# Kernel tuning notes

Hardware: AMD Instinct MI355X
Metric: run time of the kernel (lower is better)

Reference implementation:

```python
import jax, jax.numpy as jnp
import numpy as np

N_NODES = 50000
N_EDGES = 800000
D = 128            # in_channels == hidden_channels
N_LAYERS = 3
OUT = 16
N_GRAPHS = 128


def setup_inputs() -> dict:
    key = jax.random.key(0)
    ks = jax.random.split(key, 12)
    x = jax.random.normal(ks[0], (N_NODES, D), dtype=jnp.float32)
    edge_index = jax.random.randint(ks[1], (2, N_EDGES), 0, N_NODES, dtype=jnp.int64)
    batch_ids = jnp.sort(jax.random.randint(ks[2], (N_NODES,), 0, N_GRAPHS, dtype=jnp.int64))
    s = 1.0 / np.sqrt(D)
    # Stacked per-layer GraphConv weights (all layers are D->D here).
    Wrel = jax.random.uniform(ks[3], (N_LAYERS, D, D), jnp.float32, -s, s)
    brel = jax.random.uniform(ks[4], (N_LAYERS, D), jnp.float32, -s, s)
    Wroot = jax.random.uniform(ks[5], (N_LAYERS, D, D), jnp.float32, -s, s)
    # post_mp MLP head
    W1 = jax.random.uniform(ks[6], (D, D), jnp.float32, -s, s)
    b1 = jax.random.uniform(ks[7], (D,), jnp.float32, -s, s)
    W2 = jax.random.uniform(ks[8], (D, OUT), jnp.float32, -s, s)
    b2 = jax.random.uniform(ks[9], (OUT,), jnp.float32, -s, s)
    return {"x": x, "edge_index": edge_index, "batch_ids": batch_ids,
            "Wrel": Wrel, "brel": brel, "Wroot": Wroot,
            "W1": W1, "b1": b1, "W2": W2, "b2": b2}


def reference(x, edge_index, batch_ids, Wrel, brel, Wroot, W1, b1, W2, b2):
    src, dst = edge_index[0], edge_index[1]
    h = x
    for l in range(N_LAYERS):
        # GraphConv: lin_rel(sum_{j->i} h_j) + lin_root(h_i)
        agg = jax.ops.segment_sum(h[src], dst, num_segments=N_NODES)  # [N, D]
        h = agg @ Wrel[l] + brel[l] + h @ Wroot[l]
        h = jax.nn.relu(h)
        # dropout p=0.0 / eval mode -> identity
    # global mean pool over graphs
    sums = jax.ops.segment_sum(h, batch_ids, num_segments=N_GRAPHS)          # [G, D]
    counts = jax.ops.segment_sum(jnp.ones((N_NODES,), h.dtype), batch_ids,
                                 num_segments=N_GRAPHS)                       # [G]
    pooled = sums / jnp.maximum(counts, 1.0)[:, None]
    # post_mp MLP (dropout identity in eval)
    out = (pooled @ W1 + b1) @ W2 + b2                                        # [G, OUT]
    return out
```

## Files before the change

kernel.cpp:

```cpp
#include <hip/hip_runtime.h>

#define N_NODES 50000
#define N_EDGES 800000
#define D 128
#define N_LAYERS 3
#define OUT_F 16
#define N_GRAPHS 128
#define NBUCK 391
#define EPB 4096
#define NB3 ((N_EDGES + EPB - 1) / EPB)
#define CAP 4096
#define NT32 ((N_NODES + 31) / 32)
#define PITCH 132
#define NCAST 6250
#define NPREPW 96

typedef __attribute__((ext_vector_type(8))) short short8;
typedef __attribute__((ext_vector_type(16))) float floatx16;

__device__ __forceinline__ unsigned short f2bf(float f) {
  unsigned int u = __float_as_uint(f);
  u += 0x7fff + ((u >> 16) & 1);
  return (unsigned short)(u >> 16);
}
__device__ __forceinline__ float bf2f(unsigned short b) {
  return __uint_as_float(((unsigned int)b) << 16);
}
__device__ __forceinline__ float blo(unsigned v) { return __uint_as_float(v << 16); }
__device__ __forceinline__ float bhi(unsigned v) { return __uint_as_float(v & 0xffff0000u); }

__global__ __launch_bounds__(256) void prep_part_kernel(
    const int* __restrict__ src, const int* __restrict__ dst,
    int* __restrict__ cursor, unsigned* __restrict__ pairs,
    const float* __restrict__ x, unsigned short* __restrict__ x16,
    const float* __restrict__ Wrel, const float* __restrict__ Wroot,
    unsigned short* __restrict__ wt) {
  __shared__ unsigned pk[EPB];
  __shared__ int hist[NBUCK];
  __shared__ int wcur[NBUCK];
  const int bid = blockIdx.x;
  const int t = threadIdx.x;
  if (bid < NB3) {
    const int e0 = bid * EPB;
    const int n = min(EPB, N_EDGES - e0);
    for (int i = t; i < NBUCK; i += 256) hist[i] = 0;
    __syncthreads();
    for (int i = t; i < n; i += 256) {
      int d = dst[e0 + i], s = src[e0 + i];
      pk[i] = ((unsigned)d << 16) | (unsigned)s;
      atomicAdd(&hist[d >> 7], 1);
    }
    __syncthreads();
    for (int i = t; i < NBUCK; i += 256)
      wcur[i] = i * CAP + (hist[i] ? atomicAdd(&cursor[i], hist[i]) : 0);
    __syncthreads();
    for (int i = t; i < n; i += 256) {
      unsigned p = pk[i];
      int pos = atomicAdd(&wcur[p >> 23], 1);
      pairs[pos] = p;
    }
  } else if (bid < NB3 + NCAST) {
    const int i = (bid - NB3) * 256 + t;
    const float4 v = *(const float4*)&x[(size_t)i * 4];
    uint2 o;
    o.x = f2bf(v.x) | ((unsigned)f2bf(v.y) << 16);
    o.y = f2bf(v.z) | ((unsigned)f2bf(v.w) << 16);
    *(uint2*)&x16[(size_t)i * 4] = o;
  } else {
    const int idx = (bid - NB3 - NCAST) * 256 + t;
    const int lane = idx & 63;
    const int kst = (idx >> 6) & 31;
    const int nt = (idx >> 11) & 1;
    const int half = (idx >> 12) & 1;
    const int l = idx >> 13;
    const int n = half * 64 + nt * 32 + (lane & 31);
    const int kx0 = kst * 16 + (lane >> 5) * 8;
    const int seg = kx0 >> 7;
    const int k0 = kx0 & 127;
    const int mat = seg >> 1, lo = seg & 1;
    const float* W = (mat ? Wroot : Wrel) + (size_t)l * D * D;
    unsigned short v[8];
#pragma unroll
    for (int j = 0; j < 8; ++j) {
      float w = W[(size_t)(k0 + j) * D + n];
      unsigned short hi = f2bf(w);
      v[j] = lo ? f2bf(w - bf2f(hi)) : hi;
    }
    unsigned short* dstp =
        wt + ((size_t)l * 128 + (half * 2 + nt) * 32 + kst) * 512 + lane * 8;
    *(uint4*)dstp = *(const uint4*)v;
  }
}

__global__ __launch_bounds__(256) void bucket_sort_kernel(
    const unsigned* __restrict__ pairs, const int* __restrict__ cursor,
    int* __restrict__ rowbeg, int* __restrict__ rowend, int* __restrict__ esrc) {
  __shared__ unsigned pk[CAP];
  __shared__ int sorted[CAP];
  __shared__ int hist[128], off[128], cur[128];
  const int bkt = blockIdx.x;
  const int t = threadIdx.x;
  const int beg = bkt * CAP;
  const int cnt = cursor[bkt];
  if (t < 128) hist[t] = 0;
  __syncthreads();
  for (int i = t; i < cnt; i += 256) {
    unsigned p = pairs[beg + i];
    pk[i] = p;
    atomicAdd(&hist[(p >> 16) & 127], 1);
  }
  __syncthreads();
  if (t < 128) off[t] = hist[t];
  __syncthreads();
  for (int o = 1; o < 128; o <<= 1) {
    int x = (t < 128 && t >= o) ? off[t - o] : 0;
    __syncthreads();
    if (t < 128) off[t] += x;
    __syncthreads();
  }
  if (t < 128) {
    int node = bkt * 128 + t;
    if (node < N_NODES) {
      rowbeg[node] = beg + off[t] - hist[t];
      rowend[node] = beg + off[t];
    }
    cur[t] = off[t] - hist[t];
  }
  __syncthreads();
  for (int i = t; i < cnt; i += 256) {
    unsigned p = pk[i];
    int pos = atomicAdd(&cur[(p >> 16) & 127], 1);
    sorted[pos] = (int)(p & 0xFFFFu);
  }
  __syncthreads();
  for (int i = t; i < cnt; i += 256) esrc[beg + i] = sorted[i];
}

__global__ __launch_bounds__(512, 8) void layer_kernel(
    const unsigned short* __restrict__ h,
    const int* __restrict__ rowbeg, const int* __restrict__ rowend,
    const int* __restrict__ esrc,
    const unsigned short* __restrict__ wt,
    const float* __restrict__ brel,
    unsigned short* __restrict__ outp) {
  __shared__ unsigned short atile[32 * PITCH];
  __shared__ unsigned short htile[32 * PITCH];
  __shared__ float redB[4][16][64];
  const int t = threadIdx.x;
  const int r0 = blockIdx.x * 32;
  const int g = t >> 4, li = t & 15;
  const int row = r0 + g;
  const unsigned short* hp = h + (size_t)li * 8;

  if (row < N_NODES) {
    *(uint4*)&htile[g * PITCH + li * 8] =
        *(const uint4*)&h[(size_t)row * D + li * 8];
  } else {
    const uint4 z = {0, 0, 0, 0};
    *(uint4*)&htile[g * PITCH + li * 8] = z;
  }

  int beg = 0, end = 0;
  if (row < N_NODES) { beg = rowbeg[row]; end = rowend[row]; }
  float a0 = 0, a1 = 0, a2 = 0, a3 = 0, a4 = 0, a5 = 0, a6 = 0, a7 = 0;
  int e = beg;
  for (; e + 4 <= end; e += 4) {
    const int s0 = esrc[e],     s1 = esrc[e + 1];
    const int s2 = esrc[e + 2], s3 = esrc[e + 3];
    const uint4 v0 = *(const uint4*)&hp[(size_t)s0 * D];
    const uint4 v1 = *(const uint4*)&hp[(size_t)s1 * D];
    const uint4 v2 = *(const uint4*)&hp[(size_t)s2 * D];
    const uint4 v3 = *(const uint4*)&hp[(size_t)s3 * D];
    a0 += blo(v0.x) + blo(v1.x) + blo(v2.x) + blo(v3.x);
    a1 += bhi(v0.x) + bhi(v1.x) + bhi(v2.x) + bhi(v3.x);
    a2 += blo(v0.y) + blo(v1.y) + blo(v2.y) + blo(v3.y);
    a3 += bhi(v0.y) + bhi(v1.y) + bhi(v2.y) + bhi(v3.y);
    a4 += blo(v0.z) + blo(v1.z) + blo(v2.z) + blo(v3.z);
    a5 += bhi(v0.z) + bhi(v1.z) + bhi(v2.z) + bhi(v3.z);
    a6 += blo(v0.w) + blo(v1.w) + blo(v2.w) + blo(v3.w);
    a7 += bhi(v0.w) + bhi(v1.w) + bhi(v2.w) + bhi(v3.w);
  }
  for (; e < end; ++e) {
    const uint4 v0 = *(const uint4*)&hp[(size_t)esrc[e] * D];
    a0 += blo(v0.x); a1 += bhi(v0.x);
    a2 += blo(v0.y); a3 += bhi(v0.y);
    a4 += blo(v0.z); a5 += bhi(v0.z);
    a6 += blo(v0.w); a7 += bhi(v0.w);
  }
  {
    uint4 o;
    o.x = f2bf(a0) | ((unsigned)f2bf(a1) << 16);
    o.y = f2bf(a2) | ((unsigned)f2bf(a3) << 16);
    o.z = f2bf(a4) | ((unsigned)f2bf(a5) << 16);
    o.w = f2bf(a6) | ((unsigned)f2bf(a7) << 16);
    *(uint4*)&atile[g * PITCH + li * 8] = o;
  }
  __syncthreads();

  const int wave = t >> 6, lane = t & 63;
  const int p = wave & 3, chain = wave >> 2;
  const int r2 = lane & 31, hseg = lane >> 5;
  const unsigned short* tile = chain ? htile : atile;
  short8 fr[8];
#pragma unroll
  for (int i = 0; i < 8; ++i)
    fr[i] = *(const short8*)&tile[r2 * PITCH + i * 16 + hseg * 8];
  const unsigned short* ws = wt + (size_t)(p * 32 + chain * 16) * 512;
  floatx16 acc = {0.f};
#pragma unroll
  for (int k = 0; k < 16; ++k) {
    const short8 b = *(const short8*)&ws[(size_t)k * 512 + lane * 8];
    acc = __builtin_amdgcn_mfma_f32_32x32x16_bf16(fr[k & 7], b, acc, 0, 0, 0);
  }
  if (chain) {
#pragma unroll
    for (int reg = 0; reg < 16; ++reg) redB[p][reg][lane] = acc[reg];
  }
  __syncthreads();
  if (!chain) {
    const int cb = p * 32 + r2;
    const float bias = brel[cb];
#pragma unroll
    for (int reg = 0; reg < 16; ++reg) {
      const int orow = r0 + (reg & 3) + 8 * (reg >> 2) + 4 * hseg;
      if (orow < N_NODES)
        outp[(size_t)orow * D + cb] =
            f2bf(fmaxf(acc[reg] + redB[p][reg][lane] + bias, 0.f));
    }
  }
}

__device__ __forceinline__ int lb_search(const int* __restrict__ a, int n, int key) {
  int lo = 0, hi = n;
  while (lo < hi) {
    int m = (lo + hi) >> 1;
    if (a[m] < key) lo = m + 1; else hi = m;
  }
  return lo;
}

__global__ __launch_bounds__(256) void pool_head_kernel(
    const unsigned short* __restrict__ h, const int* __restrict__ batch,
    const float* __restrict__ W1, const float* __restrict__ b1,
    const float* __restrict__ W2, const float* __restrict__ b2,
    float* __restrict__ out) {
  __shared__ float sums_lds[16][128];
  __shared__ float pooled[128];
  __shared__ float hidden[128];
  __shared__ int range[2];
  const int g = blockIdx.x;
  const int t = threadIdx.x;
  if (t < 2) range[t] = lb_search(batch, N_NODES, g + t);
  __syncthreads();
  const int lo = range[0], hi = range[1];
  const int rg = t >> 4, cg = t & 15;
  float a0 = 0, a1 = 0, a2 = 0, a3 = 0, a4 = 0, a5 = 0, a6 = 0, a7 = 0;
  for (int n = lo + rg; n < hi; n += 16) {
    const uint4 v = *(const uint4*)&h[(size_t)n * D + cg * 8];
    a0 += blo(v.x); a1 += bhi(v.x);
    a2 += blo(v.y); a3 += bhi(v.y);
    a4 += blo(v.z); a5 += bhi(v.z);
    a6 += blo(v.w); a7 += bhi(v.w);
  }
  sums_lds[rg][cg * 8 + 0] = a0; sums_lds[rg][cg * 8 + 1] = a1;
  sums_lds[rg][cg * 8 + 2] = a2; sums_lds[rg][cg * 8 + 3] = a3;
  sums_lds[rg][cg * 8 + 4] = a4; sums_lds[rg][cg * 8 + 5] = a5;
  sums_lds[rg][cg * 8 + 6] = a6; sums_lds[rg][cg * 8 + 7] = a7;
  __syncthreads();
  if (t < 128) {
    float s = 0.f;
#pragma unroll
    for (int r = 0; r < 16; ++r) s += sums_lds[r][t];
    pooled[t] = s / fmaxf((float)(hi - lo), 1.f);
  }
  __syncthreads();
  if (t < 128) {
    float a = b1[t];
    for (int k = 0; k < D; ++k) a += pooled[k] * W1[k * D + t];
    hidden[t] = a;
  }
  __syncthreads();
  if (t < OUT_F) {
    float o = b2[t];
    for (int k = 0; k < D; ++k) o += hidden[k] * W2[k * OUT_F + t];
    out[(size_t)g * OUT_F + t] = o;
  }
}

extern "C" void kernel_launch(void* const* d_in, const int* in_sizes, int n_in,
                              void* d_out, int out_size, void* d_ws, size_t ws_size,
                              hipStream_t stream) {
  const float* x     = (const float*)d_in[0];
  const int*   ei    = (const int*)d_in[1];
  const int*   batch = (const int*)d_in[2];
  const float* Wrel  = (const float*)d_in[3];
  const float* brel  = (const float*)d_in[4];
  const float* Wroot = (const float*)d_in[5];
  const float* W1    = (const float*)d_in[6];
  const float* b1    = (const float*)d_in[7];
  const float* W2    = (const float*)d_in[8];
  const float* b2    = (const float*)d_in[9];
  float* out = (float*)d_out;

  const size_t ND = (size_t)N_NODES * D;
  unsigned short* bufA = (unsigned short*)d_ws;
  unsigned short* bufB = bufA + ND;
  unsigned short* bufC = bufB + ND;
  unsigned short* wt   = bufC + ND;
  int* rowbeg = (int*)(wt + (size_t)N_LAYERS * 128 * 512);
  int* rowend = rowbeg + N_NODES;
  int* esrc   = rowend + N_NODES;
  unsigned* pairs = (unsigned*)(esrc + (size_t)NBUCK * CAP);
  int* cursor = (int*)(pairs + (size_t)NBUCK * CAP);

  const int* esrc_in = ei;
  const int* edst_in = ei + N_EDGES;

  hipMemsetAsync(cursor, 0, NBUCK * sizeof(int), stream);
  prep_part_kernel<<<NB3 + NCAST + NPREPW, 256, 0, stream>>>(
      esrc_in, edst_in, cursor, pairs, x, bufC, Wrel, Wroot, wt);
  bucket_sort_kernel<<<NBUCK, 256, 0, stream>>>(pairs, cursor, rowbeg, rowend, esrc);

  const size_t WL = (size_t)128 * 512;
  layer_kernel<<<NT32, 512, 0, stream>>>(bufC, rowbeg, rowend, esrc,
                                         wt, brel, bufA);
  layer_kernel<<<NT32, 512, 0, stream>>>(bufA, rowbeg, rowend, esrc,
                                         wt + WL, brel + D, bufB);
  layer_kernel<<<NT32, 512, 0, stream>>>(bufB, rowbeg, rowend, esrc,
                                         wt + 2 * WL, brel + 2 * D, bufA);

  pool_head_kernel<<<N_GRAPHS, 256, 0, stream>>>(bufA, batch, W1, b1, W2, b2, out);
}
```

Measured before the change: 261.2 us.

## Process 64 rows per block and run full K chain per wave without reduction

Each layer block now handles 64 nodes instead of 32, with each thread gathering two rows. In the MFMA stage each wave computes the whole 256-long K reduction (agg and root parts) for a 32x32 output tile, which removes the cross-wave LDS reduction buffer and the second barrier. The intent is to halve the per-block weight loads per row and cut synchronisation. The cost is more serial gather work per thread, more LDS per block and more registers, which may lower occupancy.

```diff
diff --git a/kernel.cpp b/kernel.cpp
--- a/kernel.cpp
+++ b/kernel.cpp
@@ -10,7 +10,7 @@
 #define EPB 4096
 #define NB3 ((N_EDGES + EPB - 1) / EPB)
 #define CAP 4096
-#define NT32 ((N_NODES + 31) / 32)
+#define NT64 ((N_NODES + 63) / 64)
 #define PITCH 132
 #define NCAST 6250
 #define NPREPW 96
@@ -143,90 +143,85 @@
     const unsigned short* __restrict__ wt,
     const float* __restrict__ brel,
     unsigned short* __restrict__ outp) {
-  __shared__ unsigned short atile[32 * PITCH];
-  __shared__ unsigned short htile[32 * PITCH];
-  __shared__ float redB[4][16][64];
+  __shared__ unsigned short atile[64 * PITCH];
+  __shared__ unsigned short htile[64 * PITCH];
   const int t = threadIdx.x;
-  const int r0 = blockIdx.x * 32;
+  const int r0 = blockIdx.x * 64;
   const int g = t >> 4, li = t & 15;
-  const int row = r0 + g;
   const unsigned short* hp = h + (size_t)li * 8;
 
-  if (row < N_NODES) {
-    *(uint4*)&htile[g * PITCH + li * 8] =
-        *(const uint4*)&h[(size_t)row * D + li * 8];
-  } else {
-    const uint4 z = {0, 0, 0, 0};
-    *(uint4*)&htile[g * PITCH + li * 8] = z;
-  }
-
-  int beg = 0, end = 0;
-  if (row < N_NODES) { beg = rowbeg[row]; end = rowend[row]; }
-  float a0 = 0, a1 = 0, a2 = 0, a3 = 0, a4 = 0, a5 = 0, a6 = 0, a7 = 0;
-  int e = beg;
-  for (; e + 4 <= end; e += 4) {
-    const int s0 = esrc[e],     s1 = esrc[e + 1];
-    const int s2 = esrc[e + 2], s3 = esrc[e + 3];
-    const uint4 v0 = *(const uint4*)&hp[(size_t)s0 * D];
-    const uint4 v1 = *(const uint4*)&hp[(size_t)s1 * D];
-    const uint4 v2 = *(const uint4*)&hp[(size_t)s2 * D];
-    const uint4 v3 = *(const uint4*)&hp[(size_t)s3 * D];
-    a0 += blo(v0.x) + blo(v1.x) + blo(v2.x) + blo(v3.x);
-    a1 += bhi(v0.x) + bhi(v1.x) + bhi(v2.x) + bhi(v3.x);
-    a2 += blo(v0.y) + blo(v1.y) + blo(v2.y) + blo(v3.y);
-    a3 += bhi(v0.y) + bhi(v1.y) + bhi(v2.y) + bhi(v3.y);
-    a4 += blo(v0.z) + blo(v1.z) + blo(v2.z) + blo(v3.z);
-    a5 += bhi(v0.z) + bhi(v1.z) + bhi(v2.z) + bhi(v3.z);
-    a6 += blo(v0.w) + blo(v1.w) + blo(v2.w) + blo(v3.w);
-    a7 += bhi(v0.w) + bhi(v1.w) + bhi(v2.w) + bhi(v3.w);
-  }
-  for (; e < end; ++e) {
-    const uint4 v0 = *(const uint4*)&hp[(size_t)esrc[e] * D];
-    a0 += blo(v0.x); a1 += bhi(v0.x);
-    a2 += blo(v0.y); a3 += bhi(v0.y);
-    a4 += blo(v0.z); a5 += bhi(v0.z);
-    a6 += blo(v0.w); a7 += bhi(v0.w);
-  }
-  {
+#pragma unroll
+  for (int rr = 0; rr < 2; ++rr) {
+    const int lr = g + rr * 32;
+    const int row = r0 + lr;
+    if (row < N_NODES) {
+      *(uint4*)&htile[lr * PITCH + li * 8] =
+          *(const uint4*)&h[(size_t)row * D + li * 8];
+    } else {
+      const uint4 z = {0, 0, 0, 0};
+      *(uint4*)&htile[lr * PITCH + li * 8] = z;
+    }
+    int beg = 0, end = 0;
+    if (row < N_NODES) { beg = rowbeg[row]; end = rowend[row]; }
+    float a0 = 0, a1 = 0, a2 = 0, a3 = 0, a4 = 0, a5 = 0, a6 = 0, a7 = 0;
+    int e = beg;
+    for (; e + 4 <= end; e += 4) {
+      const int s0 = esrc[e],     s1 = esrc[e + 1];
+      const int s2 = esrc[e + 2], s3 = esrc[e + 3];
+      const uint4 v0 = *(const uint4*)&hp[(size_t)s0 * D];
+      const uint4 v1 = *(const uint4*)&hp[(size_t)s1 * D];
+      const uint4 v2 = *(const uint4*)&hp[(size_t)s2 * D];
+      const uint4 v3 = *(const uint4*)&hp[(size_t)s3 * D];
+      a0 += blo(v0.x) + blo(v1.x) + blo(v2.x) + blo(v3.x);
+      a1 += bhi(v0.x) + bhi(v1.x) + bhi(v2.x) + bhi(v3.x);
+      a2 += blo(v0.y) + blo(v1.y) + blo(v2.y) + blo(v3.y);
+      a3 += bhi(v0.y) + bhi(v1.y) + bhi(v2.y) + bhi(v3.y);
+      a4 += blo(v0.z) + blo(v1.z) + blo(v2.z) + blo(v3.z);
+      a5 += bhi(v0.z) + bhi(v1.z) + bhi(v2.z) + bhi(v3.z);
+      a6 += blo(v0.w) + blo(v1.w) + blo(v2.w) + blo(v3.w);
+      a7 += bhi(v0.w) + bhi(v1.w) + bhi(v2.w) + bhi(v3.w);
+    }
+    for (; e < end; ++e) {
+      const uint4 v0 = *(const uint4*)&hp[(size_t)esrc[e] * D];
+      a0 += blo(v0.x); a1 += bhi(v0.x);
+      a2 += blo(v0.y); a3 += bhi(v0.y);
+      a4 += blo(v0.z); a5 += bhi(v0.z);
+      a6 += blo(v0.w); a7 += bhi(v0.w);
+    }
     uint4 o;
     o.x = f2bf(a0) | ((unsigned)f2bf(a1) << 16);
     o.y = f2bf(a2) | ((unsigned)f2bf(a3) << 16);
     o.z = f2bf(a4) | ((unsigned)f2bf(a5) << 16);
     o.w = f2bf(a6) | ((unsigned)f2bf(a7) << 16);
-    *(uint4*)&atile[g * PITCH + li * 8] = o;
+    *(uint4*)&atile[lr * PITCH + li * 8] = o;
   }
   __syncthreads();
 
   const int wave = t >> 6, lane = t & 63;
-  const int p = wave & 3, chain = wave >> 2;
+  const int tl = wave & 1, p = wave >> 1;
   const int r2 = lane & 31, hseg = lane >> 5;
-  const unsigned short* tile = chain ? htile : atile;
-  short8 fr[8];
-#pragma unroll
-  for (int i = 0; i < 8; ++i)
-    fr[i] = *(const short8*)&tile[r2 * PITCH + i * 16 + hseg * 8];
-  const unsigned short* ws = wt + (size_t)(p * 32 + chain * 16) * 512;
+  const int rbase = tl * 32 + r2;
+  short8 ag[8], hh[8];
+#pragma unroll
+  for (int i = 0; i < 8; ++i) {
+    ag[i] = *(const short8*)&atile[rbase * PITCH + i * 16 + hseg * 8];
+    hh[i] = *(const short8*)&htile[rbase * PITCH + i * 16 + hseg * 8];
+  }
+  const unsigned short* ws = wt + (size_t)p * 32 * 512;
   floatx16 acc = {0.f};
 #pragma unroll
-  for (int k = 0; k < 16; ++k) {
-    const short8 b = *(const short8*)&ws[(size_t)k * 512 + lane * 8];
-    acc = __builtin_amdgcn_mfma_f32_32x32x16_bf16(fr[k & 7], b, acc, 0, 0, 0);
-  }
-  if (chain) {
-#pragma unroll
-    for (int reg = 0; reg < 16; ++reg) redB[p][reg][lane] = acc[reg];
-  }
-  __syncthreads();
-  if (!chain) {
-    const int cb = p * 32 + r2;
-    const float bias = brel[cb];
-#pragma unroll
-    for (int reg = 0; reg < 16; ++reg) {
-      const int orow = r0 + (reg & 3) + 8 * (reg >> 2) + 4 * hseg;
-      if (orow < N_NODES)
-        outp[(size_t)orow * D + cb] =
-            f2bf(fmaxf(acc[reg] + redB[p][reg][lane] + bias, 0.f));
-    }
+  for (int kst = 0; kst < 32; ++kst) {
+    const short8 af = (kst < 16) ? ag[kst & 7] : hh[kst & 7];
+    const short8 b = *(const short8*)&ws[(size_t)kst * 512 + lane * 8];
+    acc = __builtin_amdgcn_mfma_f32_32x32x16_bf16(af, b, acc, 0, 0, 0);
+  }
+  const int cb = p * 32 + r2;
+  const float bias = brel[cb];
+#pragma unroll
+  for (int reg = 0; reg < 16; ++reg) {
+    const int orow = r0 + tl * 32 + (reg & 3) + 8 * (reg >> 2) + 4 * hseg;
+    if (orow < N_NODES)
+      outp[(size_t)orow * D + cb] = f2bf(fmaxf(acc[reg] + bias, 0.f));
   }
 }
 
@@ -322,11 +317,11 @@
   bucket_sort_kernel<<<NBUCK, 256, 0, stream>>>(pairs, cursor, rowbeg, rowend, esrc);
 
   const size_t WL = (size_t)128 * 512;
-  layer_kernel<<<NT32, 512, 0, stream>>>(bufC, rowbeg, rowend, esrc,
+  layer_kernel<<<NT64, 512, 0, stream>>>(bufC, rowbeg, rowend, esrc,
                                          wt, brel, bufA);
-  layer_kernel<<<NT32, 512, 0, stream>>>(bufA, rowbeg, rowend, esrc,
+  layer_kernel<<<NT64, 512, 0, stream>>>(bufA, rowbeg, rowend, esrc,
                                          wt + WL, brel + D, bufB);
-  layer_kernel<<<NT32, 512, 0, stream>>>(bufB, rowbeg, rowend, esrc,
+  layer_kernel<<<NT64, 512, 0, stream>>>(bufB, rowbeg, rowend, esrc,
                                          wt + 2 * WL, brel + 2 * D, bufA);
 
   pool_head_kernel<<<N_GRAPHS, 256, 0, stream>>>(bufA, batch, W1, b1, W2, b2, out);
```

New measurement: 246.2 us (median of 2 runs). -5.8%, faster.
